# Kernel optimization log

Hardware: AMD Instinct MI355X
Metric: run time of the kernel (lower is better)

## Reference

```python
import jax, jax.numpy as jnp
import numpy as np

N_EMB = 1024
HEAD_SIZE = 128


def setup_inputs() -> dict:
    key = jax.random.key(0)
    k1, k2, k3, k4 = jax.random.split(key, 4)
    B, T = 8, 4096
    x = jax.random.normal(k1, (B, T, N_EMB), dtype=jnp.float32)
    # nn.Linear(n_emb, head_size, bias=False) weights have shape [head_size, n_emb]
    s = 1.0 / np.sqrt(N_EMB)
    Wq = jax.random.uniform(k2, (HEAD_SIZE, N_EMB), jnp.float32, -s, s)
    Wk = jax.random.uniform(k3, (HEAD_SIZE, N_EMB), jnp.float32, -s, s)
    Wv = jax.random.uniform(k4, (HEAD_SIZE, N_EMB), jnp.float32, -s, s)
    return {"x": x, "Wq": Wq, "Wk": Wk, "Wv": Wv}


def reference(x, Wq, Wk, Wv):
    # x: [B, T, C]; W*: [H, C]
    B, T, C = x.shape
    H = Wq.shape[0]
    q = jnp.einsum('btc,hc->bth', x, Wq)
    k = jnp.einsum('btc,hc->bth', x, Wk)
    v = jnp.einsum('btc,hc->bth', x, Wv)
    scale = H ** -0.5
    wei = jnp.einsum('bth,bsh->bts', q, k) * scale  # [B, T, T]
    # causal mask: position t attends to s <= t
    causal = jnp.arange(T)[:, None] >= jnp.arange(T)[None, :]
    wei = jnp.where(causal, wei, -jnp.inf)
    wei = jax.nn.softmax(wei, axis=-1)
    # dropout treated as identity (eval mode)
    out = jnp.einsum('bts,bsh->bth', wei, v)  # [B, T, H]
    return out
```

## Files before the change

### kernel.cpp

```cpp
#include <hip/hip_runtime.h>
#include <hip/hip_bf16.h>

typedef __bf16 bf16_t;
typedef __attribute__((ext_vector_type(8))) __bf16 bf16x8;
typedef __attribute__((ext_vector_type(4))) __bf16 bf16x4;
typedef __attribute__((ext_vector_type(4))) float f32x4;

#define MFMA16(a, b, c) __builtin_amdgcn_mfma_f32_16x16x32_bf16((a), (b), (c), 0, 0, 0)

__device__ __forceinline__ void gload_lds16(const void* g, void* l) {
    __builtin_amdgcn_global_load_lds(
        (const __attribute__((address_space(1))) void*)g,
        (__attribute__((address_space(3))) void*)l, 16, 0, 0);
}

__global__ __launch_bounds__(256, 3) void proj_qkv(
    const float* __restrict__ X,
    const float* __restrict__ W0, const float* __restrict__ W1, const float* __restrict__ W2,
    bf16_t* __restrict__ O0, bf16_t* __restrict__ O1, bf16_t* __restrict__ O2)
{
    __shared__ __align__(16) char As[128 * 128];
    __shared__ __align__(16) char Bs[128 * 128];

    const int tid = threadIdx.x;
    const int wid = tid >> 6;
    const int lane = tid & 63;
    const int l15 = lane & 15, l4 = lane >> 4;
    const int wr = wid >> 1, wc = wid & 1;
    const int m0 = blockIdx.x * 128;

    const float* W = (blockIdx.y == 0) ? W0 : (blockIdx.y == 1 ? W1 : W2);

    const int r0 = tid >> 4;
    const int kq = tid & 15;
    const int swz = ((r0 & 7) << 4);

    f32x4 acc[4][4] = {};
    float4 xr[8];

    #pragma unroll
    for (int i = 0; i < 8; ++i)
        xr[i] = *(const float4*)(X + (size_t)(m0 + r0 + i * 16) * 1024 + kq * 4);

    for (int ks = 0; ks < 16; ++ks) {
        const int kb = ks * 64;
        #pragma unroll
        for (int i = 0; i < 8; ++i) {
            const int r = r0 + i * 16;
            bf16x4 av; av[0] = (bf16_t)xr[i].x; av[1] = (bf16_t)xr[i].y;
            av[2] = (bf16_t)xr[i].z; av[3] = (bf16_t)xr[i].w;
            *(bf16x4*)(As + r * 128 + ((kq * 8) ^ swz)) = av;
        }
        #pragma unroll
        for (int i = 0; i < 8; ++i) {
            const int r = r0 + i * 16;
            float4 wa = *(const float4*)(W + (size_t)r * 1024 + kb + kq * 4);
            bf16x4 wv; wv[0] = (bf16_t)wa.x; wv[1] = (bf16_t)wa.y;
            wv[2] = (bf16_t)wa.z; wv[3] = (bf16_t)wa.w;
            *(bf16x4*)(Bs + r * 128 + ((kq * 8) ^ swz)) = wv;
        }
        __syncthreads();
        if (ks < 15) {
            #pragma unroll
            for (int i = 0; i < 8; ++i)
                xr[i] = *(const float4*)(X + (size_t)(m0 + r0 + i * 16) * 1024 + kb + 64 + kq * 4);
        }
        #pragma unroll
        for (int kk = 0; kk < 64; kk += 32) {
            const int kbyte = 2 * kk + 16 * l4;
            bf16x8 af[4], bfr[4];
            #pragma unroll
            for (int mi = 0; mi < 4; ++mi) {
                int r = wr * 64 + mi * 16 + l15;
                af[mi] = *(const bf16x8*)(As + r * 128 + (kbyte ^ ((r & 7) << 4)));
            }
            #pragma unroll
            for (int ni = 0; ni < 4; ++ni) {
                int r = wc * 64 + ni * 16 + l15;
                bfr[ni] = *(const bf16x8*)(Bs + r * 128 + (kbyte ^ ((r & 7) << 4)));
            }
            #pragma unroll
            for (int mi = 0; mi < 4; ++mi)
                #pragma unroll
                for (int ni = 0; ni < 4; ++ni)
                    acc[mi][ni] = MFMA16(af[mi], bfr[ni], acc[mi][ni]);
        }
        __syncthreads();
    }

    if (blockIdx.y < 2) {
        const float sc = (blockIdx.y == 0) ? 0.12751754816f : 1.0f;
        bf16_t* O = (blockIdx.y == 0) ? O0 : O1;
        #pragma unroll
        for (int mi = 0; mi < 4; ++mi)
            #pragma unroll
            for (int ni = 0; ni < 4; ++ni) {
                int row = m0 + wr * 64 + mi * 16 + l4 * 4;
                int col = wc * 64 + ni * 16 + l15;
                #pragma unroll
                for (int r = 0; r < 4; ++r)
                    O[(size_t)(row + r) * 128 + col] = (bf16_t)(acc[mi][ni][r] * sc);
            }
    } else {
        #pragma unroll
        for (int mi = 0; mi < 4; ++mi)
            #pragma unroll
            for (int ni = 0; ni < 4; ++ni) {
                int row0 = m0 + wr * 64 + mi * 16 + l4 * 4;
                int col = wc * 64 + ni * 16 + l15;
                int bb = row0 >> 12, t0 = row0 & 4095;
                bf16x4 pk;
                #pragma unroll
                for (int r = 0; r < 4; ++r) pk[r] = (bf16_t)acc[mi][ni][r];
                *(bf16x4*)(O2 + ((size_t)bb << 19) + (size_t)col * 4096 + t0) = pk;
            }
    }
}

__global__ __launch_bounds__(256, 2) void attn_fwd(
    const bf16_t* __restrict__ Qb, const bf16_t* __restrict__ Kb,
    const bf16_t* __restrict__ Vtg, float* __restrict__ out, int Bn)
{
    __shared__ __align__(16) char lds[69632];

    const int tid = threadIdx.x, wid = tid >> 6, lane = tid & 63;
    const int l15 = lane & 15, l4 = lane >> 4;
    const int pair = wid >> 1, qh = wid & 1;

    const int blk = blockIdx.x;
    const int b = blk % Bn;
    const int j = blk / Bn;

    const size_t base = (size_t)b * 4096 * 128;
    const size_t baseVT = (size_t)b << 19;

    char* Pw = lds + 65536 + wid * 1024;
    const int kkey = l15 & 7;
    const int vkey = (l15 >> 1) & 3;

    bf16x8 aones;
    #pragma unroll
    for (int e = 0; e < 8; ++e) aones[e] = (bf16_t)1.0f;

    for (int seg = 0; seg < 2; ++seg) {
        const int p = seg ? (127 - j) : j;
        const int q0 = p << 5;
        const int T = p + 1;
        const int smax = (T + 1) >> 1;
        const int qg = q0 + 16 * qh + l15;

        bf16x8 aq[4];
        #pragma unroll
        for (int kf = 0; kf < 4; ++kf)
            aq[kf] = *(const bf16x8*)(Qb + base + (size_t)qg * 128 + 32 * kf + 8 * l4);

        float mx = -1e30f;
        f32x4 ls_acc = (f32x4){0.f, 0.f, 0.f, 0.f};
        f32x4 o[8] = {};

        auto stage = [&](int s) {
            const int lt = 2 * s + pair;
            if (lt >= T) return;
            const int kv0 = lt << 5;
            if (qh == 0) {
                char* Kd = lds + pair * 16384 + (s & 1) * 8192;
                #pragma unroll
                for (int c = 0; c < 8; ++c) {
                    const int row = c * 4 + (lane >> 4);
                    const bf16_t* src = Kb + base + (size_t)(kv0 + row) * 128
                                        + (((lane & 15) ^ (row & 7)) << 3);
                    gload_lds16(src, Kd + c * 1024);
                }
            } else {
                char* Vd = lds + 32768 + pair * 16384 + (s & 1) * 8192;
                #pragma unroll
                for (int c = 0; c < 8; ++c) {
                    const int row = c * 16 + (lane >> 2);
                    const bf16_t* src = Vtg + baseVT + (size_t)row * 4096 + kv0
                                        + (((lane & 3) ^ ((lane >> 3) & 3)) << 3);
                    gload_lds16(src, Vd + c * 1024);
                }
            }
        };

        __syncthreads();
        stage(0);
        __syncthreads();

        for (int s = 0; s < smax; ++s) {
            if (s + 1 < smax) stage(s + 1);
            const int lt = 2 * s + pair;
            if (lt < T) {
                const int kv0 = lt << 5;
                char* Kbuf = lds + pair * 16384 + (s & 1) * 8192;
                char* Vbuf = lds + 32768 + pair * 16384 + (s & 1) * 8192;

                f32x4 sa[2];
                #pragma unroll
                for (int ni = 0; ni < 2; ++ni) sa[ni] = (f32x4){0.f, 0.f, 0.f, 0.f};
                __builtin_amdgcn_s_setprio(1);
                #pragma unroll
                for (int kf = 0; kf < 4; ++kf)
                    #pragma unroll
                    for (int ni = 0; ni < 2; ++ni) {
                        bf16x8 ak = *(const bf16x8*)(Kbuf + (16 * ni + l15) * 256
                                                     + (((4 * kf + l4) ^ kkey) << 4));
                        sa[ni] = MFMA16(ak, aq[kf], sa[ni]);
                    }
                __builtin_amdgcn_s_setprio(0);

                if (lt == T - 1) {
                    #pragma unroll
                    for (int ni = 0; ni < 2; ++ni)
                        #pragma unroll
                        for (int r = 0; r < 4; ++r)
                            if (kv0 + 16 * ni + 4 * l4 + r > qg) sa[ni][r] = -1e30f;
                }

                float tm = fmaxf(fmaxf(fmaxf(sa[0][0], sa[0][1]),
                                       fmaxf(sa[0][2], sa[0][3])),
                                 fmaxf(fmaxf(sa[1][0], sa[1][1]),
                                       fmaxf(sa[1][2], sa[1][3])));
                if (__any(tm > mx + 8.0f)) {
                    tm = fmaxf(tm, __shfl_xor(tm, 16, 64));
                    tm = fmaxf(tm, __shfl_xor(tm, 32, 64));
                    const float mnew = fmaxf(mx, tm);
                    const float c = exp2f(mx - mnew);
                    ls_acc[0] *= c; ls_acc[1] *= c; ls_acc[2] *= c; ls_acc[3] *= c;
                    #pragma unroll
                    for (int mf = 0; mf < 8; ++mf) {
                        f32x4 t = o[mf];
                        t[0] *= c; t[1] *= c; t[2] *= c; t[3] *= c;
                        o[mf] = t;
                    }
                    mx = mnew;
                }
                #pragma unroll
                for (int ni = 0; ni < 2; ++ni) {
                    bf16x4 pv;
                    #pragma unroll
                    for (int r = 0; r < 4; ++r)
                        pv[r] = (bf16_t)exp2f(sa[ni][r] - mx);
                    *(bf16x4*)(Pw + l15 * 64
                               + (((2 * ni + (l4 >> 1)) ^ vkey) << 4) + 8 * (l4 & 1)) = pv;
                }

                bf16x8 pb = *(const bf16x8*)(Pw + l15 * 64 + ((l4 ^ vkey) << 4));
                __builtin_amdgcn_s_setprio(1);
                ls_acc = MFMA16(aones, pb, ls_acc);
                #pragma unroll
                for (int mf = 0; mf < 8; ++mf) {
                    bf16x8 av = *(const bf16x8*)(Vbuf + (16 * mf + l15) * 64
                                                 + ((l4 ^ vkey) << 4));
                    o[mf] = MFMA16(av, pb, o[mf]);
                }
                __builtin_amdgcn_s_setprio(0);
            }
            __syncthreads();
        }

        __syncthreads();
        if (pair == 1) {
            char* dst = lds + qh * 8192;
            #pragma unroll
            for (int mf = 0; mf < 8; ++mf)
                *(f32x4*)(dst + mf * 1024 + lane * 16) = o[mf];
            *(float2*)(lds + 49152 + qh * 512 + lane * 8) = make_float2(mx, ls_acc[0]);
        }
        __syncthreads();
        if (pair == 0) {
            float2 st = *(const float2*)(lds + 49152 + qh * 512 + lane * 8);
            const float mB = st.x, lB = st.y;
            const float M = fmaxf(mx, mB);
            const float a = exp2f(mx - M), b2 = exp2f(mB - M);
            const float linv = 1.f / (ls_acc[0] * a + lB * b2);
            char* srcO = lds + qh * 8192;
            float* op = out + ((size_t)b * 4096 + qg) * 128 + 4 * l4;
            #pragma unroll
            for (int mf = 0; mf < 8; ++mf) {
                f32x4 ob = *(const f32x4*)(srcO + mf * 1024 + lane * 16);
                f32x4 r;
                #pragma unroll
                for (int e = 0; e < 4; ++e) r[e] = (o[mf][e] * a + ob[e] * b2) * linv;
                *(f32x4*)(op + 16 * mf) = r;
            }
        }
    }
}

extern "C" void kernel_launch(void* const* d_in, const int* in_sizes, int n_in,
                              void* d_out, int out_size, void* d_ws, size_t ws_size,
                              hipStream_t stream) {
    const float* X  = (const float*)d_in[0];
    const float* Wq = (const float*)d_in[1];
    const float* Wk = (const float*)d_in[2];
    const float* Wv = (const float*)d_in[3];
    float* out = (float*)d_out;

    const int M = in_sizes[0] / 1024;
    const int Bn = M / 4096;

    bf16_t* Qb  = (bf16_t*)d_ws;
    bf16_t* KbP = Qb + (size_t)M * 128;
    bf16_t* VtP = KbP + (size_t)M * 128;

    proj_qkv<<<dim3(M / 128, 3), 256, 0, stream>>>(X, Wq, Wk, Wv, Qb, KbP, VtP);
    attn_fwd<<<dim3(64 * Bn), 256, 0, stream>>>(Qb, KbP, VtP, out, Bn);
}
```

Before: 128.3 us.

## Convert weights to bf16 once and widen attention blocks to 64 query rows

A small new kernel converts the three fp32 weight matrices to bf16 once per call. The projection kernel can then load bf16x8 weight chunks directly instead of converting fp32 on every tile load. The attention kernel now uses 512-thread blocks covering 64 query rows with 4 query sub-groups sharing each K/V tile, which halves the number of blocks and the K/V load traffic per query. The stage loads are split across more waves, and the per-step causal bounds check is removed. In exchange there is an extra kernel launch, heavier LDS use and larger blocks, which may lower occupancy.

After: 125.4 us. -2.3%, faster.

```diff
diff --git a/kernel.cpp b/kernel.cpp
--- a/kernel.cpp
+++ b/kernel.cpp
@@ -14,9 +14,21 @@
         (__attribute__((address_space(3))) void*)l, 16, 0, 0);
 }
 
+__global__ __launch_bounds__(256) void conv_w(
+    const float* __restrict__ W0, const float* __restrict__ W1,
+    const float* __restrict__ W2, bf16_t* __restrict__ Wb)
+{
+    const int idx = blockIdx.x * 256 + threadIdx.x;
+    const float* src = (idx < 32768) ? W0 : (idx < 65536) ? W1 : W2;
+    const int off = (idx & 32767) * 4;
+    float4 v = *(const float4*)(src + off);
+    bf16x4 o; o[0] = (bf16_t)v.x; o[1] = (bf16_t)v.y;
+    o[2] = (bf16_t)v.z; o[3] = (bf16_t)v.w;
+    *(bf16x4*)(Wb + (size_t)idx * 4) = o;
+}
+
 __global__ __launch_bounds__(256, 3) void proj_qkv(
-    const float* __restrict__ X,
-    const float* __restrict__ W0, const float* __restrict__ W1, const float* __restrict__ W2,
+    const float* __restrict__ X, const bf16_t* __restrict__ Wb,
     bf16_t* __restrict__ O0, bf16_t* __restrict__ O1, bf16_t* __restrict__ O2)
 {
     __shared__ __align__(16) char As[128 * 128];
@@ -29,7 +41,7 @@
     const int wr = wid >> 1, wc = wid & 1;
     const int m0 = blockIdx.x * 128;
 
-    const float* W = (blockIdx.y == 0) ? W0 : (blockIdx.y == 1 ? W1 : W2);
+    const bf16_t* Wp = Wb + (size_t)blockIdx.y * 131072;
 
     const int r0 = tid >> 4;
     const int kq = tid & 15;
@@ -52,12 +64,11 @@
             *(bf16x4*)(As + r * 128 + ((kq * 8) ^ swz)) = av;
         }
         #pragma unroll
-        for (int i = 0; i < 8; ++i) {
-            const int r = r0 + i * 16;
-            float4 wa = *(const float4*)(W + (size_t)r * 1024 + kb + kq * 4);
-            bf16x4 wv; wv[0] = (bf16_t)wa.x; wv[1] = (bf16_t)wa.y;
-            wv[2] = (bf16_t)wa.z; wv[3] = (bf16_t)wa.w;
-            *(bf16x4*)(Bs + r * 128 + ((kq * 8) ^ swz)) = wv;
+        for (int i = 0; i < 4; ++i) {
+            const int c = i * 256 + tid;
+            const int row = c >> 3, ch = c & 7;
+            bf16x8 wv = *(const bf16x8*)(Wp + (size_t)row * 1024 + kb + ch * 8);
+            *(bf16x8*)(Bs + row * 128 + ((ch ^ (row & 7)) << 4)) = wv;
         }
         __syncthreads();
         if (ks < 15) {
@@ -117,15 +128,15 @@
     }
 }
 
-__global__ __launch_bounds__(256, 2) void attn_fwd(
+__global__ __launch_bounds__(512, 4) void attn_fwd(
     const bf16_t* __restrict__ Qb, const bf16_t* __restrict__ Kb,
     const bf16_t* __restrict__ Vtg, float* __restrict__ out, int Bn)
 {
-    __shared__ __align__(16) char lds[69632];
+    __shared__ __align__(16) char lds[73728];
 
     const int tid = threadIdx.x, wid = tid >> 6, lane = tid & 63;
     const int l15 = lane & 15, l4 = lane >> 4;
-    const int pair = wid >> 1, qh = wid & 1;
+    const int qh = wid >> 1, pair = wid & 1;
 
     const int blk = blockIdx.x;
     const int b = blk % Bn;
@@ -143,10 +154,9 @@
     for (int e = 0; e < 8; ++e) aones[e] = (bf16_t)1.0f;
 
     for (int seg = 0; seg < 2; ++seg) {
-        const int p = seg ? (127 - j) : j;
-        const int q0 = p << 5;
-        const int T = p + 1;
-        const int smax = (T + 1) >> 1;
+        const int p = seg ? (63 - j) : j;
+        const int q0 = p << 6;
+        const int smax = p + 1;
         const int qg = q0 + 16 * qh + l15;
 
         bf16x8 aq[4];
@@ -160,25 +170,26 @@
 
         auto stage = [&](int s) {
             const int lt = 2 * s + pair;
-            if (lt >= T) return;
             const int kv0 = lt << 5;
-            if (qh == 0) {
+            if (qh < 2) {
                 char* Kd = lds + pair * 16384 + (s & 1) * 8192;
                 #pragma unroll
-                for (int c = 0; c < 8; ++c) {
-                    const int row = c * 4 + (lane >> 4);
+                for (int c = 0; c < 4; ++c) {
+                    const int it = qh * 4 + c;
+                    const int row = it * 4 + (lane >> 4);
                     const bf16_t* src = Kb + base + (size_t)(kv0 + row) * 128
                                         + (((lane & 15) ^ (row & 7)) << 3);
-                    gload_lds16(src, Kd + c * 1024);
+                    gload_lds16(src, Kd + it * 1024);
                 }
             } else {
                 char* Vd = lds + 32768 + pair * 16384 + (s & 1) * 8192;
                 #pragma unroll
-                for (int c = 0; c < 8; ++c) {
-                    const int row = c * 16 + (lane >> 2);
+                for (int c = 0; c < 4; ++c) {
+                    const int it = (qh - 2) * 4 + c;
+                    const int row = it * 16 + (lane >> 2);
                     const bf16_t* src = Vtg + baseVT + (size_t)row * 4096 + kv0
                                         + (((lane & 3) ^ ((lane >> 3) & 3)) << 3);
-                    gload_lds16(src, Vd + c * 1024);
+                    gload_lds16(src, Vd + it * 1024);
                 }
             }
         };
@@ -190,86 +201,84 @@
         for (int s = 0; s < smax; ++s) {
             if (s + 1 < smax) stage(s + 1);
             const int lt = 2 * s + pair;
-            if (lt < T) {
-                const int kv0 = lt << 5;
-                char* Kbuf = lds + pair * 16384 + (s & 1) * 8192;
-                char* Vbuf = lds + 32768 + pair * 16384 + (s & 1) * 8192;
-
-                f32x4 sa[2];
-                #pragma unroll
-                for (int ni = 0; ni < 2; ++ni) sa[ni] = (f32x4){0.f, 0.f, 0.f, 0.f};
-                __builtin_amdgcn_s_setprio(1);
-                #pragma unroll
-                for (int kf = 0; kf < 4; ++kf)
-                    #pragma unroll
-                    for (int ni = 0; ni < 2; ++ni) {
-                        bf16x8 ak = *(const bf16x8*)(Kbuf + (16 * ni + l15) * 256
-                                                     + (((4 * kf + l4) ^ kkey) << 4));
-                        sa[ni] = MFMA16(ak, aq[kf], sa[ni]);
-                    }
-                __builtin_amdgcn_s_setprio(0);
-
-                if (lt == T - 1) {
-                    #pragma unroll
-                    for (int ni = 0; ni < 2; ++ni)
-                        #pragma unroll
-                        for (int r = 0; r < 4; ++r)
-                            if (kv0 + 16 * ni + 4 * l4 + r > qg) sa[ni][r] = -1e30f;
+            const int kv0 = lt << 5;
+            char* Kbuf = lds + pair * 16384 + (s & 1) * 8192;
+            char* Vbuf = lds + 32768 + pair * 16384 + (s & 1) * 8192;
+
+            f32x4 sa[2];
+            #pragma unroll
+            for (int ni = 0; ni < 2; ++ni) sa[ni] = (f32x4){0.f, 0.f, 0.f, 0.f};
+            __builtin_amdgcn_s_setprio(1);
+            #pragma unroll
+            for (int kf = 0; kf < 4; ++kf)
+                #pragma unroll
+                for (int ni = 0; ni < 2; ++ni) {
+                    bf16x8 ak = *(const bf16x8*)(Kbuf + (16 * ni + l15) * 256
+                                                 + (((4 * kf + l4) ^ kkey) << 4));
+                    sa[ni] = MFMA16(ak, aq[kf], sa[ni]);
                 }
-
-                float tm = fmaxf(fmaxf(fmaxf(sa[0][0], sa[0][1]),
-                                       fmaxf(sa[0][2], sa[0][3])),
-                                 fmaxf(fmaxf(sa[1][0], sa[1][1]),
-                                       fmaxf(sa[1][2], sa[1][3])));
-                if (__any(tm > mx + 8.0f)) {
-                    tm = fmaxf(tm, __shfl_xor(tm, 16, 64));
-                    tm = fmaxf(tm, __shfl_xor(tm, 32, 64));
-                    const float mnew = fmaxf(mx, tm);
-                    const float c = exp2f(mx - mnew);
-                    ls_acc[0] *= c; ls_acc[1] *= c; ls_acc[2] *= c; ls_acc[3] *= c;
-                    #pragma unroll
-                    for (int mf = 0; mf < 8; ++mf) {
-                        f32x4 t = o[mf];
-                        t[0] *= c; t[1] *= c; t[2] *= c; t[3] *= c;
-                        o[mf] = t;
-                    }
-                    mx = mnew;
-                }
-                #pragma unroll
-                for (int ni = 0; ni < 2; ++ni) {
-                    bf16x4 pv;
+            __builtin_amdgcn_s_setprio(0);
+
+            if (lt >= 2 * p) {
+                #pragma unroll
+                for (int ni = 0; ni < 2; ++ni)
                     #pragma unroll
                     for (int r = 0; r < 4; ++r)
-                        pv[r] = (bf16_t)exp2f(sa[ni][r] - mx);
-                    *(bf16x4*)(Pw + l15 * 64
-                               + (((2 * ni + (l4 >> 1)) ^ vkey) << 4) + 8 * (l4 & 1)) = pv;
+                        if (kv0 + 16 * ni + 4 * l4 + r > qg) sa[ni][r] = -1e30f;
+            }
+
+            float tm = fmaxf(fmaxf(fmaxf(sa[0][0], sa[0][1]),
+                                   fmaxf(sa[0][2], sa[0][3])),
+                             fmaxf(fmaxf(sa[1][0], sa[1][1]),
+                                   fmaxf(sa[1][2], sa[1][3])));
+            if (__any(tm > mx + 8.0f)) {
+                tm = fmaxf(tm, __shfl_xor(tm, 16, 64));
+                tm = fmaxf(tm, __shfl_xor(tm, 32, 64));
+                const float mnew = fmaxf(mx, tm);
+                const float c = exp2f(mx - mnew);
+                ls_acc[0] *= c; ls_acc[1] *= c; ls_acc[2] *= c; ls_acc[3] *= c;
+                #pragma unroll
+                for (int mf = 0; mf < 8; ++mf) {
+                    f32x4 t = o[mf];
+                    t[0] *= c; t[1] *= c; t[2] *= c; t[3] *= c;
+                    o[mf] = t;
                 }
-
-                bf16x8 pb = *(const bf16x8*)(Pw + l15 * 64 + ((l4 ^ vkey) << 4));
-                __builtin_amdgcn_s_setprio(1);
-                ls_acc = MFMA16(aones, pb, ls_acc);
-                #pragma unroll
-                for (int mf = 0; mf < 8; ++mf) {
-                    bf16x8 av = *(const bf16x8*)(Vbuf + (16 * mf + l15) * 64
-                                                 + ((l4 ^ vkey) << 4));
-                    o[mf] = MFMA16(av, pb, o[mf]);
-                }
-                __builtin_amdgcn_s_setprio(0);
-            }
+                mx = mnew;
+            }
+            #pragma unroll
+            for (int ni = 0; ni < 2; ++ni) {
+                bf16x4 pv;
+                #pragma unroll
+                for (int r = 0; r < 4; ++r)
+                    pv[r] = (bf16_t)exp2f(sa[ni][r] - mx);
+                *(bf16x4*)(Pw + l15 * 64
+                           + (((2 * ni + (l4 >> 1)) ^ vkey) << 4) + 8 * (l4 & 1)) = pv;
+            }
+
+            bf16x8 pb = *(const bf16x8*)(Pw + l15 * 64 + ((l4 ^ vkey) << 4));
+            __builtin_amdgcn_s_setprio(1);
+            ls_acc = MFMA16(aones, pb, ls_acc);
+            #pragma unroll
+            for (int mf = 0; mf < 8; ++mf) {
+                bf16x8 av = *(const bf16x8*)(Vbuf + (16 * mf + l15) * 64
+                                             + ((l4 ^ vkey) << 4));
+                o[mf] = MFMA16(av, pb, o[mf]);
+            }
+            __builtin_amdgcn_s_setprio(0);
+
             __syncthreads();
         }
 
-        __syncthreads();
         if (pair == 1) {
             char* dst = lds + qh * 8192;
             #pragma unroll
             for (int mf = 0; mf < 8; ++mf)
                 *(f32x4*)(dst + mf * 1024 + lane * 16) = o[mf];
-            *(float2*)(lds + 49152 + qh * 512 + lane * 8) = make_float2(mx, ls_acc[0]);
+            *(float2*)(lds + 32768 + qh * 512 + lane * 8) = make_float2(mx, ls_acc[0]);
         }
         __syncthreads();
         if (pair == 0) {
-            float2 st = *(const float2*)(lds + 49152 + qh * 512 + lane * 8);
+            float2 st = *(const float2*)(lds + 32768 + qh * 512 + lane * 8);
             const float mB = st.x, lB = st.y;
             const float M = fmaxf(mx, mB);
             const float a = exp2f(mx - M), b2 = exp2f(mB - M);
@@ -303,7 +312,9 @@
     bf16_t* Qb  = (bf16_t*)d_ws;
     bf16_t* KbP = Qb + (size_t)M * 128;
     bf16_t* VtP = KbP + (size_t)M * 128;
-
-    proj_qkv<<<dim3(M / 128, 3), 256, 0, stream>>>(X, Wq, Wk, Wv, Qb, KbP, VtP);
-    attn_fwd<<<dim3(64 * Bn), 256, 0, stream>>>(Qb, KbP, VtP, out, Bn);
-}
+    bf16_t* Wb  = VtP + (size_t)M * 128;
+
+    conv_w<<<dim3(384), 256, 0, stream>>>(Wq, Wk, Wv, Wb);
+    proj_qkv<<<dim3(M / 128, 3), 256, 0, stream>>>(X, Wb, Qb, KbP, VtP);
+    attn_fwd<<<dim3(32 * Bn), 512, 0, stream>>>(Qb, KbP, VtP, out, Bn);
+}
```
